# Performance work log

Hardware: AMD Instinct MI355X
Metric: run time of the kernel (lower is better)

Reference implementation:

```python
import jax, jax.numpy as jnp
import numpy as np

B, N, C_IN, C_H, C_OUT, R, X_DIM = 32, 256, 64, 128, 128, 5, 1024
NEG = -9e15

def _leaky(x, s=0.2):
    return jnp.where(x >= 0, x, s * x)

def gat_layer(atoms, mask, W, b, a):
    # atoms: (B,n,c_in), mask: (B,n,n,R) bool, W: (c_in, R*c), b: (R*c,), a: (R, 2c)
    bs, n, _ = atoms.shape
    c = a.shape[1] // 2
    h = (atoms @ W + b).reshape(bs, n, R, c)            # (B,n,R,c)
    src = jnp.einsum('bnrc,rc->bnr', h, a[:, :c])       # a . h_i part
    dst = jnp.einsum('bnrc,rc->bnr', h, a[:, c:])       # a . h_j part
    logits = _leaky(src[:, :, None, :] + dst[:, None, :, :])  # (B,i,j,R)
    masked = jnp.where(mask, logits, NEG)
    probs = jax.nn.softmax(masked.reshape(bs, n, n * R), axis=2).reshape(bs, n, n, R)
    return jnp.einsum('bijr,bjrc->bic', probs, h)       # (B,n,c)

def setup_inputs() -> dict:
    key = jax.random.key(0)
    ks = jax.random.split(key, 16)
    def p(k, shape, fan):
        return jax.random.normal(k, shape, jnp.float32) * (1.414 / np.sqrt(fan))
    inp = {
        'x': jax.random.normal(ks[0], (B, X_DIM), jnp.float32),
        'y_atoms': jax.random.normal(ks[1], (B, N, C_IN), jnp.float32),
        'y_bonds': jax.random.randint(ks[2], (B, N, N, R), 0, 2, jnp.int32),
        'W1': p(ks[3], (C_IN, R * C_H), C_IN), 'b1': jnp.zeros((R * C_H,), jnp.float32),
        'a1': p(ks[4], (R, 2 * C_H), 2 * C_H),
        'W2': p(ks[5], (C_H, R * C_H), C_H), 'b2': jnp.zeros((R * C_H,), jnp.float32),
        'a2': p(ks[6], (R, 2 * C_H), 2 * C_H),
        'W3': p(ks[7], (C_H, R * C_OUT), C_H), 'b3': jnp.zeros((R * C_OUT,), jnp.float32),
        'a3': p(ks[8], (R, 2 * C_OUT), 2 * C_OUT),
        'We1': p(ks[9], (2 * C_OUT + X_DIM, 256), 2 * C_OUT + X_DIM), 'be1': jnp.zeros((256,), jnp.float32),
        'We2': p(ks[10], (256, 32), 256), 'be2': jnp.zeros((32,), jnp.float32),
        'We3': p(ks[11], (32, 1), 32), 'be3': jnp.zeros((1,), jnp.float32),
    }
    return inp

def reference(x, y_atoms, y_bonds, W1, b1, a1, W2, b2, a2, W3, b3, a3,
              We1, be1, We2, be2, We3, be3):
    mask = (y_bonds == 1)
    h = gat_layer(y_atoms, mask, W1, b1, a1)
    h = _leaky(h)                                   # dropout is identity at eval
    h = gat_layer(h, mask, W2, b2, a2)
    h = _leaky(h)
    h = gat_layer(h, mask, W3, b3, a3)
    y_feats = jnp.concatenate([jnp.mean(h, axis=1), jnp.max(h, axis=1)], axis=1)
    z = jnp.concatenate([x, y_feats], axis=1)
    z = _leaky(z @ We1 + be1)
    z = _leaky(z @ We2 + be2)
    return z @ We3 + be3
```

## Files before the change

kernel.cpp:

```cpp
#include <hip/hip_runtime.h>
#include <cstddef>

#define BB 32
#define NN 256
#define RR 5

typedef __attribute__((ext_vector_type(8))) short bf16x8;
typedef __attribute__((ext_vector_type(4))) float f32x4;

__device__ __forceinline__ float lrelu(float x) { return x >= 0.f ? x : 0.2f * x; }
__device__ __forceinline__ unsigned short f2bf(float x) {
    unsigned u = __float_as_uint(x);
    u += 0x7FFFu + ((u >> 16) & 1u);
    return (unsigned short)(u >> 16);
}

__global__ __launch_bounds__(256) void k_prep(const float* __restrict__ W1,
                                              const float* __restrict__ W2,
                                              const float* __restrict__ W3,
                                              const float* __restrict__ We1,
                                              const int* __restrict__ bonds,
                                              unsigned short* __restrict__ WT1,
                                              unsigned short* __restrict__ WT2,
                                              unsigned short* __restrict__ WT3,
                                              float* __restrict__ We1T,
                                              unsigned char* __restrict__ maskp) {
    __shared__ float Ls[40][256];
    int blk = blockIdx.x;
    int t = threadIdx.x;
    if (blk < 30) {
        int layer = blk / 10, nt = blk % 10;
        const float* W;
        unsigned short* WT;
        int K;
        if (layer == 0)      { W = W1; WT = WT1; K = 64; }
        else if (layer == 1) { W = W2; WT = WT2; K = 128; }
        else                 { W = W3; WT = WT3; K = 128; }
        int n = nt * 64 + (t & 63);
        for (int kg = (int)(t >> 6); kg < K / 8; kg += 4) {
            bf16x8 v;
#pragma unroll
            for (int e = 0; e < 8; ++e) v[e] = (short)f2bf(W[(size_t)(kg * 8 + e) * 640 + n]);
            *(bf16x8*)&WT[(size_t)n * K + kg * 8] = v;
        }
    } else if (blk < 62) {
        int bt = blk - 30;
        for (int kk = 0; kk < 40; ++kk)
            Ls[kk][t] = We1[(size_t)(bt * 40 + kk) * 256 + t];
        __syncthreads();
#pragma unroll
        for (int q = 0; q < 10; ++q) {
            float4 v;
            v.x = Ls[q * 4 + 0][t]; v.y = Ls[q * 4 + 1][t];
            v.z = Ls[q * 4 + 2][t]; v.w = Ls[q * 4 + 3][t];
            *(float4*)&We1T[(size_t)t * 1280 + bt * 40 + q * 4] = v;
        }
    } else {
        int idx = (blk - 62) * 256 + t;
        const int* p = bonds + (size_t)idx * 5;
        unsigned m = 0;
#pragma unroll
        for (int r = 0; r < 5; ++r) m |= (p[r] == 1) ? (1u << r) : 0u;
        maskp[idx] = (unsigned char)m;
    }
}

template <int K, bool ABF16>
__global__ __launch_bounds__(256) void k_gemm_h(const float* __restrict__ Af32,
                                                const unsigned short* __restrict__ Abf,
                                                const unsigned short* __restrict__ WTg,
                                                const float* __restrict__ bias,
                                                const float* __restrict__ avec,
                                                float* __restrict__ srcp,
                                                float* __restrict__ dstp,
                                                unsigned short* __restrict__ hTf) {
    const int t = threadIdx.x;
    const int n0 = blockIdx.x * 64, m0 = blockIdx.y * 64;
    const int w = t >> 6, lane = t & 63;
    const int colg = lane & 15, rquad = lane >> 4;
    const int m = m0 + w * 16 + colg;
    const int koff = rquad * 8;

    f32x4 acc[4] = {};
#pragma unroll
    for (int kk = 0; kk < K; kk += 32) {
        bf16x8 af;
        if (ABF16) {
            af = *(const bf16x8*)&Abf[(size_t)m * K + kk + koff];
        } else {
            size_t off = (size_t)m * K + kk + koff;
            float4 q0 = *(const float4*)&Af32[off];
            float4 q1 = *(const float4*)&Af32[off + 4];
            af[0] = (short)f2bf(q0.x); af[1] = (short)f2bf(q0.y);
            af[2] = (short)f2bf(q0.z); af[3] = (short)f2bf(q0.w);
            af[4] = (short)f2bf(q1.x); af[5] = (short)f2bf(q1.y);
            af[6] = (short)f2bf(q1.z); af[7] = (short)f2bf(q1.w);
        }
#pragma unroll
        for (int ct = 0; ct < 4; ++ct) {
            bf16x8 bfv = *(const bf16x8*)&WTg[(size_t)(n0 + ct * 16 + colg) * K + kk + koff];
            acc[ct] = __builtin_amdgcn_mfma_f32_16x16x32_bf16(af, bfv, acc[ct], 0, 0, 0);
        }
    }

    const int r = n0 >> 7, chalf = n0 & 127;
    const int b = m0 >> 8, jb = m0 & 255;
    float val[4][4];
    float ssum[4] = {0.f, 0.f, 0.f, 0.f}, dsum[4] = {0.f, 0.f, 0.f, 0.f};
#pragma unroll
    for (int ct = 0; ct < 4; ++ct) {
        int cg = chalf + ct * 16 + colg;
        float bv = bias[n0 + ct * 16 + colg];
        float asr = avec[r * 256 + cg];
        float ads = avec[r * 256 + 128 + cg];
#pragma unroll
        for (int reg = 0; reg < 4; ++reg) {
            float v = acc[ct][reg] + bv;
            val[ct][reg] = v;
            ssum[reg] += v * asr;
            dsum[reg] += v * ads;
        }
    }
#pragma unroll
    for (int mk = 1; mk < 16; mk <<= 1)
#pragma unroll
        for (int reg = 0; reg < 4; ++reg) {
            ssum[reg] += __shfl_xor(ssum[reg], mk);
            dsum[reg] += __shfl_xor(dsum[reg], mk);
        }
    if (colg == 0) {
        int half = (n0 >> 6) & 1;
#pragma unroll
        for (int reg = 0; reg < 4; ++reg) {
            int row = m0 + w * 16 + rquad * 4 + reg;
            srcp[half * 40960 + row * 5 + r] = ssum[reg];
            dstp[half * 40960 + row * 5 + r] = dsum[reg];
        }
    }
    {
        const int joct = (jb >> 3) + w * 2 + (rquad >> 1);
        const size_t tile = (size_t)((b * 5 + r) * 32 + joct) * 1024;
        const int sub = (rquad & 1) * 4;
#pragma unroll
        for (int ct = 0; ct < 4; ++ct) {
            int c = chalf + ct * 16 + colg;
            uint2 pk;
            pk.x = (unsigned)f2bf(val[ct][0]) | ((unsigned)f2bf(val[ct][1]) << 16);
            pk.y = (unsigned)f2bf(val[ct][2]) | ((unsigned)f2bf(val[ct][3]) << 16);
            *(uint2*)&hTf[tile + (size_t)c * 8 + sub] = pk;
        }
    }
}

template <bool LAST>
__global__ __launch_bounds__(256) void k_agg(const unsigned short* __restrict__ hTf,
                                             const float* __restrict__ srcp,
                                             const float* __restrict__ dstp,
                                             const unsigned char* __restrict__ maskp,
                                             unsigned short* __restrict__ Abf,
                                             float* __restrict__ poolS,
                                             float* __restrict__ poolM) {
    __shared__ unsigned short Ps[40 * 64 * 8];
    __shared__ float Ss[80], Ds2[1280], Zrow[16], Zi[16];
    __shared__ float Os[16][132];
    const int t = threadIdx.x;
    const int itile = blockIdx.x, b = blockIdx.y;
    const int ib = b * 256 + itile * 16;

    if (t < 80) Ss[t] = srcp[(size_t)ib * 5 + t] + srcp[40960 + (size_t)ib * 5 + t];
    if (t >= 80 && t < 96) Zrow[t - 80] = 0.f;
    for (int idx = t; idx < 1280; idx += 256) {
        int jl = idx & 255, rr = idx >> 8;
        size_t o = (size_t)(b * 256 + jl) * 5 + rr;
        Ds2[rr * 256 + jl] = dstp[o] + dstp[40960 + o];
    }
    __syncthreads();

    const int i_mine = t & 15;
    {
        float sv5[5];
#pragma unroll
        for (int r = 0; r < 5; ++r) sv5[r] = Ss[i_mine * 5 + r];
        float esum = 0.f;
#pragma unroll
        for (int it = 0; it < 10; ++it) {
            int p = it * 256 + t;
            int lane8 = p & 63, s = p >> 6;
            int kq = lane8 >> 4;
            int k0 = s * 32 + kq * 8;
            int rr = k0 >> 8, j0 = k0 & 255;
            uint2 mk8 = *(const uint2*)&maskp[((size_t)(ib + i_mine) << 8) + j0];
            float sv = sv5[rr];
            bf16x8 pv;
#pragma unroll
            for (int e = 0; e < 8; ++e) {
                unsigned mb = ((e < 4 ? (mk8.x >> (8 * e)) : (mk8.y >> (8 * (e - 4)))) >> rr) & 1u;
                float v = lrelu(sv + Ds2[k0 + e]);
                float ev = mb ? __expf(v) : 0.f;
                unsigned short q = f2bf(ev);
                pv[e] = (short)q;
                esum += __uint_as_float((unsigned)q << 16);
            }
            *(bf16x8*)&Ps[p * 8] = pv;
        }
        atomicAdd(&Zrow[i_mine], esum);
    }
    __syncthreads();
    if (t < 16) Zi[t] = 1.f / Zrow[t];
    __syncthreads();

    const int w = t >> 6, lane = t & 63;
    const int colg = lane & 15, rquad = lane >> 4;
    f32x4 acc[2] = {};
    const size_t bbase = (size_t)(b * 5) * 32 * 1024;
#pragma unroll
    for (int s = 0; s < 40; ++s) {
        bf16x8 af = *(const bf16x8*)&Ps[(s * 64 + lane) * 8];
        const size_t tbase = bbase + (size_t)((s >> 3) * 32 + (s & 7) * 4 + rquad) * 1024;
#pragma unroll
        for (int ct = 0; ct < 2; ++ct) {
            int c = w * 32 + ct * 16 + colg;
            bf16x8 bfv = *(const bf16x8*)&hTf[tbase + (size_t)c * 8];
            acc[ct] = __builtin_amdgcn_mfma_f32_16x16x32_bf16(af, bfv, acc[ct], 0, 0, 0);
        }
    }
    __syncthreads();
#pragma unroll
    for (int ct = 0; ct < 2; ++ct) {
        int c = w * 32 + ct * 16 + colg;
#pragma unroll
        for (int reg = 0; reg < 4; ++reg) {
            int i = rquad * 4 + reg;
            Os[i][c] = acc[ct][reg] * Zi[i];
        }
    }
    __syncthreads();

    if (!LAST) {
        int i = t >> 4, c0 = (t & 15) * 8;
        bf16x8 ob;
#pragma unroll
        for (int e = 0; e < 8; ++e) ob[e] = (short)f2bf(lrelu(Os[i][c0 + e]));
        *(bf16x8*)&Abf[(size_t)(ib + i) * 128 + c0] = ob;
    } else {
        if (t < 128) {
            float sm = 0.f, mx = -3.4e38f;
#pragma unroll
            for (int i = 0; i < 16; ++i) {
                float v = Os[i][t];
                sm += v; mx = fmaxf(mx, v);
            }
            poolS[(b * 16 + itile) * 128 + t] = sm;
            poolM[(b * 16 + itile) * 128 + t] = mx;
        }
    }
}

__global__ __launch_bounds__(256) void k_mlp1(const float* __restrict__ x,
                                              const float* __restrict__ poolS,
                                              const float* __restrict__ poolM,
                                              const float* __restrict__ We1T,
                                              const float* __restrict__ be1,
                                              float* __restrict__ z1g) {
    int og = blockIdx.x, b = blockIdx.y;
    int t = threadIdx.x;
    __shared__ float zs[1280];
    for (int i = t; i < 1024; i += 256) zs[i] = x[b * 1024 + i];
    if (t < 128) {
        float s = 0.f;
#pragma unroll
        for (int nc = 0; nc < 16; ++nc) s += poolS[(b * 16 + nc) * 128 + t];
        zs[1024 + t] = s * (1.f / 256.f);
    } else {
        int f = t - 128;
        float mx = -3.4e38f;
#pragma unroll
        for (int nc = 0; nc < 16; ++nc) mx = fmaxf(mx, poolM[(b * 16 + nc) * 128 + f]);
        zs[1152 + f] = mx;
    }
    __syncthreads();
    int w = t >> 6, lane = t & 63;
#pragma unroll
    for (int oo = 0; oo < 4; ++oo) {
        int o = og * 16 + w * 4 + oo;
        float s = 0.f;
#pragma unroll
        for (int i = 0; i < 20; ++i) {
            int k = i * 64 + lane;
            s += zs[k] * We1T[(size_t)o * 1280 + k];
        }
#pragma unroll
        for (int off = 32; off > 0; off >>= 1) s += __shfl_down(s, off);
        if (lane == 0) z1g[b * 256 + o] = lrelu(s + be1[o]);
    }
}

__global__ __launch_bounds__(256) void k_mlp23(const float* __restrict__ z1g,
                                               const float* __restrict__ We2,
                                               const float* __restrict__ be2,
                                               const float* __restrict__ We3,
                                               const float* __restrict__ be3,
                                               float* __restrict__ out) {
    int b = blockIdx.x, t = threadIdx.x;
    __shared__ float zs[256], z2s[32];
    zs[t] = z1g[b * 256 + t];
    __syncthreads();
    if (t < 32) {
        float s2 = be2[t];
        for (int k = 0; k < 256; ++k) s2 += zs[k] * We2[k * 32 + t];
        z2s[t] = lrelu(s2);
    }
    __syncthreads();
    if (t == 0) {
        float s3 = be3[0];
#pragma unroll
        for (int k = 0; k < 32; ++k) s3 += z2s[k] * We3[k];
        out[b] = s3;
    }
}

constexpr size_t O_MASK  = 0;
constexpr size_t O_SRCP  = 2097152;
constexpr size_t O_DSTP  = O_SRCP + 2ull * 40960 * 4;
constexpr size_t O_ABF   = O_DSTP + 2ull * 40960 * 4;
constexpr size_t O_HT    = O_ABF + 1048576ull * 2;
constexpr size_t O_WT1   = O_HT + 5242880ull * 2;
constexpr size_t O_WT2   = O_WT1 + 640ull * 64 * 2;
constexpr size_t O_WT3   = O_WT2 + 640ull * 128 * 2;
constexpr size_t O_WE1T  = O_WT3 + 640ull * 128 * 2;
constexpr size_t O_POOLS = O_WE1T + 256ull * 1280 * 4;
constexpr size_t O_POOLM = O_POOLS + 32ull * 16 * 128 * 4;
constexpr size_t O_Z1    = O_POOLM + 32ull * 16 * 128 * 4;

extern "C" void kernel_launch(void* const* d_in, const int* in_sizes, int n_in,
                              void* d_out, int out_size, void* d_ws, size_t ws_size,
                              hipStream_t stream) {
    const float* x       = (const float*)d_in[0];
    const float* y_atoms = (const float*)d_in[1];
    const int*   y_bonds = (const int*)d_in[2];
    const float* W1 = (const float*)d_in[3];
    const float* b1 = (const float*)d_in[4];
    const float* a1 = (const float*)d_in[5];
    const float* W2 = (const float*)d_in[6];
    const float* b2 = (const float*)d_in[7];
    const float* a2 = (const float*)d_in[8];
    const float* W3 = (const float*)d_in[9];
    const float* b3 = (const float*)d_in[10];
    const float* a3 = (const float*)d_in[11];
    const float* We1 = (const float*)d_in[12];
    const float* be1 = (const float*)d_in[13];
    const float* We2 = (const float*)d_in[14];
    const float* be2 = (const float*)d_in[15];
    const float* We3 = (const float*)d_in[16];
    const float* be3 = (const float*)d_in[17];
    float* out = (float*)d_out;

    char* ws = (char*)d_ws;
    unsigned char* maskp = (unsigned char*)(ws + O_MASK);
    float* srcp = (float*)(ws + O_SRCP);
    float* dstp = (float*)(ws + O_DSTP);
    unsigned short* Abf = (unsigned short*)(ws + O_ABF);
    unsigned short* hTf = (unsigned short*)(ws + O_HT);
    unsigned short* WT1 = (unsigned short*)(ws + O_WT1);
    unsigned short* WT2 = (unsigned short*)(ws + O_WT2);
    unsigned short* WT3 = (unsigned short*)(ws + O_WT3);
    float* We1T  = (float*)(ws + O_WE1T);
    float* poolS = (float*)(ws + O_POOLS);
    float* poolM = (float*)(ws + O_POOLM);
    float* z1g   = (float*)(ws + O_Z1);

    dim3 blk(256);

    k_prep<<<8254, blk, 0, stream>>>(W1, W2, W3, We1, y_bonds, WT1, WT2, WT3, We1T, maskp);

    k_gemm_h<64, false><<<dim3(10, 128), blk, 0, stream>>>(
        y_atoms, nullptr, WT1, b1, a1, srcp, dstp, hTf);
    k_agg<false><<<dim3(16, 32), blk, 0, stream>>>(hTf, srcp, dstp, maskp, Abf, nullptr, nullptr);

    k_gemm_h<128, true><<<dim3(10, 128), blk, 0, stream>>>(
        nullptr, Abf, WT2, b2, a2, srcp, dstp, hTf);
    k_agg<false><<<dim3(16, 32), blk, 0, stream>>>(hTf, srcp, dstp, maskp, Abf, nullptr, nullptr);

    k_gemm_h<128, true><<<dim3(10, 128), blk, 0, stream>>>(
        nullptr, Abf, WT3, b3, a3, srcp, dstp, hTf);
    k_agg<true><<<dim3(16, 32), blk, 0, stream>>>(hTf, srcp, dstp, maskp, nullptr, poolS, poolM);

    k_mlp1<<<dim3(16, 32), blk, 0, stream>>>(x, poolS, poolM, We1T, be1, z1g);
    k_mlp23<<<32, blk, 0, stream>>>(z1g, We2, be2, We3, be3, out);
}
```

Measured before the change: 228.2 us.

## Split aggregation over j halves and defer normalization into next GEMM and MLP

The aggregation kernel now splits the neighbour dimension into two halves and processes 32 rows per 512-thread block. Each half writes unnormalized fp32 partial sums plus partial softmax denominators. The following GEMM sums the two partials, normalizes, applies leaky ReLU and converts to bf16 in its A-load, and the pooling and three MLP layers are fused into one kernel. This gives each block less serial MFMA work and removes a launch, at the cost of writing and reading twice as much fp32 intermediate data instead of bf16.

```diff
diff --git a/kernel.cpp b/kernel.cpp
--- a/kernel.cpp
+++ b/kernel.cpp
@@ -65,9 +65,10 @@
     }
 }
 
-template <int K, bool ABF16>
+template <int K, int MODE>
 __global__ __launch_bounds__(256) void k_gemm_h(const float* __restrict__ Af32,
-                                                const unsigned short* __restrict__ Abf,
+                                                const float* __restrict__ aggP,
+                                                const float* __restrict__ Zpart,
                                                 const unsigned short* __restrict__ WTg,
                                                 const float* __restrict__ bias,
                                                 const float* __restrict__ avec,
@@ -81,14 +82,28 @@
     const int m = m0 + w * 16 + colg;
     const int koff = rquad * 8;
 
+    float zi = 0.f;
+    if (MODE == 1) zi = 1.f / (Zpart[m] + Zpart[8192 + m]);
+
     f32x4 acc[4] = {};
 #pragma unroll
     for (int kk = 0; kk < K; kk += 32) {
         bf16x8 af;
-        if (ABF16) {
-            af = *(const bf16x8*)&Abf[(size_t)m * K + kk + koff];
+        size_t off = (size_t)m * K + kk + koff;
+        if (MODE == 1) {
+            float4 a0 = *(const float4*)&aggP[off];
+            float4 a1 = *(const float4*)&aggP[off + 4];
+            float4 b0 = *(const float4*)&aggP[off + 1048576];
+            float4 b1 = *(const float4*)&aggP[off + 1048576 + 4];
+            af[0] = (short)f2bf(lrelu((a0.x + b0.x) * zi));
+            af[1] = (short)f2bf(lrelu((a0.y + b0.y) * zi));
+            af[2] = (short)f2bf(lrelu((a0.z + b0.z) * zi));
+            af[3] = (short)f2bf(lrelu((a0.w + b0.w) * zi));
+            af[4] = (short)f2bf(lrelu((a1.x + b1.x) * zi));
+            af[5] = (short)f2bf(lrelu((a1.y + b1.y) * zi));
+            af[6] = (short)f2bf(lrelu((a1.z + b1.z) * zi));
+            af[7] = (short)f2bf(lrelu((a1.w + b1.w) * zi));
         } else {
-            size_t off = (size_t)m * K + kk + koff;
             float4 q0 = *(const float4*)&Af32[off];
             float4 q1 = *(const float4*)&Af32[off + 4];
             af[0] = (short)f2bf(q0.x); af[1] = (short)f2bf(q0.y);
@@ -152,162 +167,137 @@
     }
 }
 
-template <bool LAST>
-__global__ __launch_bounds__(256) void k_agg(const unsigned short* __restrict__ hTf,
+__global__ __launch_bounds__(512) void k_agg(const unsigned short* __restrict__ hTf,
                                              const float* __restrict__ srcp,
                                              const float* __restrict__ dstp,
                                              const unsigned char* __restrict__ maskp,
-                                             unsigned short* __restrict__ Abf,
-                                             float* __restrict__ poolS,
-                                             float* __restrict__ poolM) {
-    __shared__ unsigned short Ps[40 * 64 * 8];
-    __shared__ float Ss[80], Ds2[1280], Zrow[16], Zi[16];
-    __shared__ float Os[16][132];
+                                             float* __restrict__ aggP,
+                                             float* __restrict__ Zpart) {
+    __shared__ unsigned short Ps[20480];
+    __shared__ float Ss[160], Ds2l[640], Zrow[32];
     const int t = threadIdx.x;
-    const int itile = blockIdx.x, b = blockIdx.y;
-    const int ib = b * 256 + itile * 16;
-
-    if (t < 80) Ss[t] = srcp[(size_t)ib * 5 + t] + srcp[40960 + (size_t)ib * 5 + t];
-    if (t >= 80 && t < 96) Zrow[t - 80] = 0.f;
-    for (int idx = t; idx < 1280; idx += 256) {
-        int jl = idx & 255, rr = idx >> 8;
-        size_t o = (size_t)(b * 256 + jl) * 5 + rr;
-        Ds2[rr * 256 + jl] = dstp[o] + dstp[40960 + o];
-    }
-    __syncthreads();
-
-    const int i_mine = t & 15;
-    {
-        float sv5[5];
-#pragma unroll
-        for (int r = 0; r < 5; ++r) sv5[r] = Ss[i_mine * 5 + r];
+    const int js = blockIdx.x, itile = blockIdx.y, b = blockIdx.z;
+    const int ib = b * 256 + itile * 32;
+
+    if (t < 160) Ss[t] = srcp[(size_t)ib * 5 + t] + srcp[40960 + (size_t)ib * 5 + t];
+    if (t >= 160 && t < 192) Zrow[t - 160] = 0.f;
+    for (int idx = t; idx < 640; idx += 512) {
+        int jl = idx & 127, rr = idx >> 7;
+        size_t o = (size_t)(b * 256 + js * 128 + jl) * 5 + rr;
+        Ds2l[rr * 128 + jl] = dstp[o] + dstp[40960 + o];
+    }
+    __syncthreads();
+
+#pragma unroll
+    for (int it = 0; it < 5; ++it) {
+        int p = it * 512 + t;
+        int lane8 = p & 63, chunkrow = p >> 6;
+        int colg8 = lane8 & 15, kq = lane8 >> 4;
+        int ih = (chunkrow >= 20) ? 1 : 0;
+        int s = chunkrow - ih * 20;
+        int i = ih * 16 + colg8;
+        int rr = s >> 2;
+        int j0l = (s & 3) * 32 + kq * 8;
+        uint2 mk8 = *(const uint2*)&maskp[((size_t)(ib + i) << 8) + js * 128 + j0l];
+        float sv = Ss[i * 5 + rr];
         float esum = 0.f;
-#pragma unroll
-        for (int it = 0; it < 10; ++it) {
-            int p = it * 256 + t;
-            int lane8 = p & 63, s = p >> 6;
-            int kq = lane8 >> 4;
-            int k0 = s * 32 + kq * 8;
-            int rr = k0 >> 8, j0 = k0 & 255;
-            uint2 mk8 = *(const uint2*)&maskp[((size_t)(ib + i_mine) << 8) + j0];
-            float sv = sv5[rr];
-            bf16x8 pv;
-#pragma unroll
-            for (int e = 0; e < 8; ++e) {
-                unsigned mb = ((e < 4 ? (mk8.x >> (8 * e)) : (mk8.y >> (8 * (e - 4)))) >> rr) & 1u;
-                float v = lrelu(sv + Ds2[k0 + e]);
-                float ev = mb ? __expf(v) : 0.f;
-                unsigned short q = f2bf(ev);
-                pv[e] = (short)q;
-                esum += __uint_as_float((unsigned)q << 16);
-            }
-            *(bf16x8*)&Ps[p * 8] = pv;
-        }
-        atomicAdd(&Zrow[i_mine], esum);
-    }
-    __syncthreads();
-    if (t < 16) Zi[t] = 1.f / Zrow[t];
-    __syncthreads();
+        bf16x8 pv;
+#pragma unroll
+        for (int e = 0; e < 8; ++e) {
+            unsigned mb = ((e < 4 ? (mk8.x >> (8 * e)) : (mk8.y >> (8 * (e - 4)))) >> rr) & 1u;
+            float v = lrelu(sv + Ds2l[rr * 128 + j0l + e]);
+            float ev = mb ? __expf(v) : 0.f;
+            unsigned short q = f2bf(ev);
+            pv[e] = (short)q;
+            esum += __uint_as_float((unsigned)q << 16);
+        }
+        *(bf16x8*)&Ps[p * 8] = pv;
+        atomicAdd(&Zrow[i], esum);
+    }
+    __syncthreads();
+    if (t < 32) Zpart[(size_t)js * 8192 + ib + t] = Zrow[t];
 
     const int w = t >> 6, lane = t & 63;
+    const int ih = w & 1, ch = w >> 1;
     const int colg = lane & 15, rquad = lane >> 4;
     f32x4 acc[2] = {};
     const size_t bbase = (size_t)(b * 5) * 32 * 1024;
 #pragma unroll
-    for (int s = 0; s < 40; ++s) {
-        bf16x8 af = *(const bf16x8*)&Ps[(s * 64 + lane) * 8];
-        const size_t tbase = bbase + (size_t)((s >> 3) * 32 + (s & 7) * 4 + rquad) * 1024;
+    for (int s = 0; s < 20; ++s) {
+        bf16x8 af = *(const bf16x8*)&Ps[((ih * 20 + s) * 64 + lane) * 8];
+        const int rr = s >> 2;
+        const int joct = js * 16 + (s & 3) * 4 + rquad;
+        const size_t tbase = bbase + (size_t)(rr * 32 + joct) * 1024;
 #pragma unroll
         for (int ct = 0; ct < 2; ++ct) {
-            int c = w * 32 + ct * 16 + colg;
+            int c = ch * 32 + ct * 16 + colg;
             bf16x8 bfv = *(const bf16x8*)&hTf[tbase + (size_t)c * 8];
             acc[ct] = __builtin_amdgcn_mfma_f32_16x16x32_bf16(af, bfv, acc[ct], 0, 0, 0);
         }
     }
-    __syncthreads();
+    float* op = aggP + (size_t)js * 1048576;
+    const int irow = ib + ih * 16 + rquad * 4;
 #pragma unroll
     for (int ct = 0; ct < 2; ++ct) {
-        int c = w * 32 + ct * 16 + colg;
-#pragma unroll
-        for (int reg = 0; reg < 4; ++reg) {
-            int i = rquad * 4 + reg;
-            Os[i][c] = acc[ct][reg] * Zi[i];
-        }
-    }
-    __syncthreads();
-
-    if (!LAST) {
-        int i = t >> 4, c0 = (t & 15) * 8;
-        bf16x8 ob;
-#pragma unroll
-        for (int e = 0; e < 8; ++e) ob[e] = (short)f2bf(lrelu(Os[i][c0 + e]));
-        *(bf16x8*)&Abf[(size_t)(ib + i) * 128 + c0] = ob;
-    } else {
-        if (t < 128) {
-            float sm = 0.f, mx = -3.4e38f;
-#pragma unroll
-            for (int i = 0; i < 16; ++i) {
-                float v = Os[i][t];
-                sm += v; mx = fmaxf(mx, v);
-            }
-            poolS[(b * 16 + itile) * 128 + t] = sm;
-            poolM[(b * 16 + itile) * 128 + t] = mx;
-        }
-    }
-}
-
-__global__ __launch_bounds__(256) void k_mlp1(const float* __restrict__ x,
-                                              const float* __restrict__ poolS,
-                                              const float* __restrict__ poolM,
-                                              const float* __restrict__ We1T,
-                                              const float* __restrict__ be1,
-                                              float* __restrict__ z1g) {
-    int og = blockIdx.x, b = blockIdx.y;
-    int t = threadIdx.x;
-    __shared__ float zs[1280];
-    for (int i = t; i < 1024; i += 256) zs[i] = x[b * 1024 + i];
+        int c = ch * 32 + ct * 16 + colg;
+#pragma unroll
+        for (int reg = 0; reg < 4; ++reg)
+            op[(size_t)(irow + reg) * 128 + c] = acc[ct][reg];
+    }
+}
+
+__global__ __launch_bounds__(512) void k_mlp(const float* __restrict__ x,
+                                             const float* __restrict__ aggP,
+                                             const float* __restrict__ Zpart,
+                                             const float* __restrict__ We1T,
+                                             const float* __restrict__ be1,
+                                             const float* __restrict__ We2,
+                                             const float* __restrict__ be2,
+                                             const float* __restrict__ We3,
+                                             const float* __restrict__ be3,
+                                             float* __restrict__ out) {
+    int b = blockIdx.x, t = threadIdx.x;
+    __shared__ float zs[1280], Zi[256], S4[4][128], M4[4][128], z1s[256], z2s[32];
+
+    if (t < 256) {
+        int rowg = b * 256 + t;
+        Zi[t] = 1.f / (Zpart[rowg] + Zpart[8192 + rowg]);
+    }
+    for (int i = t; i < 1024; i += 512) zs[i] = x[b * 1024 + i];
+    __syncthreads();
+    {
+        int c = t & 127, grp = t >> 7;
+        float sm = 0.f, mx = -3.4e38f;
+#pragma unroll
+        for (int nn = 0; nn < 64; ++nn) {
+            int n = grp * 64 + nn;
+            size_t o = (size_t)(b * 256 + n) * 128 + c;
+            float v = (aggP[o] + aggP[o + 1048576]) * Zi[n];
+            sm += v; mx = fmaxf(mx, v);
+        }
+        S4[grp][c] = sm; M4[grp][c] = mx;
+    }
+    __syncthreads();
     if (t < 128) {
-        float s = 0.f;
-#pragma unroll
-        for (int nc = 0; nc < 16; ++nc) s += poolS[(b * 16 + nc) * 128 + t];
-        zs[1024 + t] = s * (1.f / 256.f);
-    } else {
+        zs[1024 + t] = (S4[0][t] + S4[1][t] + S4[2][t] + S4[3][t]) * (1.f / 256.f);
+    } else if (t < 256) {
         int f = t - 128;
-        float mx = -3.4e38f;
-#pragma unroll
-        for (int nc = 0; nc < 16; ++nc) mx = fmaxf(mx, poolM[(b * 16 + nc) * 128 + f]);
-        zs[1152 + f] = mx;
-    }
-    __syncthreads();
-    int w = t >> 6, lane = t & 63;
-#pragma unroll
-    for (int oo = 0; oo < 4; ++oo) {
-        int o = og * 16 + w * 4 + oo;
-        float s = 0.f;
-#pragma unroll
-        for (int i = 0; i < 20; ++i) {
-            int k = i * 64 + lane;
-            s += zs[k] * We1T[(size_t)o * 1280 + k];
-        }
-#pragma unroll
-        for (int off = 32; off > 0; off >>= 1) s += __shfl_down(s, off);
-        if (lane == 0) z1g[b * 256 + o] = lrelu(s + be1[o]);
-    }
-}
-
-__global__ __launch_bounds__(256) void k_mlp23(const float* __restrict__ z1g,
-                                               const float* __restrict__ We2,
-                                               const float* __restrict__ be2,
-                                               const float* __restrict__ We3,
-                                               const float* __restrict__ be3,
-                                               float* __restrict__ out) {
-    int b = blockIdx.x, t = threadIdx.x;
-    __shared__ float zs[256], z2s[32];
-    zs[t] = z1g[b * 256 + t];
+        zs[1152 + f] = fmaxf(fmaxf(M4[0][f], M4[1][f]), fmaxf(M4[2][f], M4[3][f]));
+    }
+    __syncthreads();
+    if (t < 256) {
+        float s = be1[t];
+        const float* wr = &We1T[(size_t)t * 1280];
+        for (int k = 0; k < 1280; k += 4) {
+            float4 wv = *(const float4*)&wr[k];
+            s += zs[k] * wv.x + zs[k + 1] * wv.y + zs[k + 2] * wv.z + zs[k + 3] * wv.w;
+        }
+        z1s[t] = lrelu(s);
+    }
     __syncthreads();
     if (t < 32) {
         float s2 = be2[t];
-        for (int k = 0; k < 256; ++k) s2 += zs[k] * We2[k * 32 + t];
+        for (int k = 0; k < 256; ++k) s2 += z1s[k] * We2[k * 32 + t];
         z2s[t] = lrelu(s2);
     }
     __syncthreads();
@@ -322,15 +312,13 @@
 constexpr size_t O_MASK  = 0;
 constexpr size_t O_SRCP  = 2097152;
 constexpr size_t O_DSTP  = O_SRCP + 2ull * 40960 * 4;
-constexpr size_t O_ABF   = O_DSTP + 2ull * 40960 * 4;
-constexpr size_t O_HT    = O_ABF + 1048576ull * 2;
+constexpr size_t O_AGG   = O_DSTP + 2ull * 40960 * 4;
+constexpr size_t O_ZP    = O_AGG + 2ull * 1048576 * 4;
+constexpr size_t O_HT    = O_ZP + 2ull * 8192 * 4;
 constexpr size_t O_WT1   = O_HT + 5242880ull * 2;
 constexpr size_t O_WT2   = O_WT1 + 640ull * 64 * 2;
 constexpr size_t O_WT3   = O_WT2 + 640ull * 128 * 2;
 constexpr size_t O_WE1T  = O_WT3 + 640ull * 128 * 2;
-constexpr size_t O_POOLS = O_WE1T + 256ull * 1280 * 4;
-constexpr size_t O_POOLM = O_POOLS + 32ull * 16 * 128 * 4;
-constexpr size_t O_Z1    = O_POOLM + 32ull * 16 * 128 * 4;
 
 extern "C" void kernel_launch(void* const* d_in, const int* in_sizes, int n_in,
                               void* d_out, int out_size, void* d_ws, size_t ws_size,
@@ -359,32 +347,29 @@
     unsigned char* maskp = (unsigned char*)(ws + O_MASK);
     float* srcp = (float*)(ws + O_SRCP);
     float* dstp = (float*)(ws + O_DSTP);
-    unsigned short* Abf = (unsigned short*)(ws + O_ABF);
+    float* aggP = (float*)(ws + O_AGG);
+    float* Zpart = (float*)(ws + O_ZP);
     unsigned short* hTf = (unsigned short*)(ws + O_HT);
     unsigned short* WT1 = (unsigned short*)(ws + O_WT1);
     unsigned short* WT2 = (unsigned short*)(ws + O_WT2);
     unsigned short* WT3 = (unsigned short*)(ws + O_WT3);
     float* We1T  = (float*)(ws + O_WE1T);
-    float* poolS = (float*)(ws + O_POOLS);
-    float* poolM = (float*)(ws + O_POOLM);
-    float* z1g   = (float*)(ws + O_Z1);
 
     dim3 blk(256);
 
     k_prep<<<8254, blk, 0, stream>>>(W1, W2, W3, We1, y_bonds, WT1, WT2, WT3, We1T, maskp);
 
-    k_gemm_h<64, false><<<dim3(10, 128), blk, 0, stream>>>(
-        y_atoms, nullptr, WT1, b1, a1, srcp, dstp, hTf);
-    k_agg<false><<<dim3(16, 32), blk, 0, stream>>>(hTf, srcp, dstp, maskp, Abf, nullptr, nullptr);
-
-    k_gemm_h<128, true><<<dim3(10, 128), blk, 0, stream>>>(
-        nullptr, Abf, WT2, b2, a2, srcp, dstp, hTf);
-    k_agg<false><<<dim3(16, 32), blk, 0, stream>>>(hTf, srcp, dstp, maskp, Abf, nullptr, nullptr);
-
-    k_gemm_h<128, true><<<dim3(10, 128), blk, 0, stream>>>(
-        nullptr, Abf, WT3, b3, a3, srcp, dstp, hTf);
-    k_agg<true><<<dim3(16, 32), blk, 0, stream>>>(hTf, srcp, dstp, maskp, nullptr, poolS, poolM);
-
-    k_mlp1<<<dim3(16, 32), blk, 0, stream>>>(x, poolS, poolM, We1T, be1, z1g);
-    k_mlp23<<<32, blk, 0, stream>>>(z1g, We2, be2, We3, be3, out);
-}
+    k_gemm_h<64, 0><<<dim3(10, 128), blk, 0, stream>>>(
+        y_atoms, nullptr, nullptr, WT1, b1, a1, srcp, dstp, hTf);
+    k_agg<<<dim3(2, 8, 32), dim3(512), 0, stream>>>(hTf, srcp, dstp, maskp, aggP, Zpart);
+
+    k_gemm_h<128, 1><<<dim3(10, 128), blk, 0, stream>>>(
+        nullptr, aggP, Zpart, WT2, b2, a2, srcp, dstp, hTf);
+    k_agg<<<dim3(2, 8, 32), dim3(512), 0, stream>>>(hTf, srcp, dstp, maskp, aggP, Zpart);
+
+    k_gemm_h<128, 1><<<dim3(10, 128), blk, 0, stream>>>(
+        nullptr, aggP, Zpart, WT3, b3, a3, srcp, dstp, hTf);
+    k_agg<<<dim3(2, 8, 32), dim3(512), 0, stream>>>(hTf, srcp, dstp, maskp, aggP, Zpart);
+
+    k_mlp<<<32, dim3(512), 0, stream>>>(x, aggP, Zpart, We1T, be1, We2, be2, We3, be3, out);
+}
```

Result: slower. 264.4 us (+15.9%).
